# Kernel optimization log

Measured on AMD Instinct MI355X. Metric: run time of the kernel, lower is better.

Reference implementation:

```python
import jax, jax.numpy as jnp
import numpy as np

B, N, K = 4, 65536, 16
D_IN, D_OUT = 8, 16
DH = D_OUT // 2
GROUPS = 4  # GroupNorm: 4 groups since all channel counts here are < 64
NEG = 0.2   # LeakyReLU negative slope
EPS = 1e-5  # GroupNorm eps (torch default)


def _gather(feat, idx):
    # feat [B,C,N], idx [B,N,K] -> [B,C,N,K]  (gather_neighbour_V2)
    return jax.vmap(lambda f, i: f[:, i])(feat, idx)


def _gn(x, gamma, beta):
    b, c, n, k = x.shape
    xg = x.reshape(b, GROUPS, c // GROUPS, n, k)
    mu = xg.mean(axis=(2, 3, 4), keepdims=True)
    var = xg.var(axis=(2, 3, 4), keepdims=True)
    xg = (xg - mu) * jax.lax.rsqrt(var + EPS)
    return xg.reshape(b, c, n, k) * gamma[None, :, None, None] + beta[None, :, None, None]


def _mlp2d(x, W, bb, g, be, act=True):
    # Conv2d 1x1 (+bias) + GroupNorm + optional LeakyReLU(0.2)
    y = jnp.einsum('oc,bcnk->bonk', W, x) + bb[None, :, None, None]
    y = _gn(y, g, be)
    return jax.nn.leaky_relu(y, NEG) if act else y


def _att_pool(x, Wa, Wm, bm, gm, bem):
    # Att_pooling: 1x1 fc (no bias) -> softmax over nsample -> weighted sum -> MLP2D
    scores = jax.nn.softmax(jnp.einsum('oc,bcnk->bonk', Wa, x), axis=3)
    agg = jnp.sum(x * scores, axis=3, keepdims=True)  # [B,C,N,1]
    return _mlp2d(agg, Wm, bm, gm, bem)


def setup_inputs():
    key = jax.random.key(0)
    ks = list(jax.random.split(key, 16))
    def w(k, o, c):
        return jax.random.normal(k, (o, c), jnp.float32) * (2.0 / c) ** 0.5  # kaiming-ish
    inp = {
        'feature': jax.random.normal(ks[0], (B, D_IN, N, 1), jnp.float32),
        'xyz': jax.random.normal(ks[1], (B, 3, N), jnp.float32),
        'neigh_idx': jax.random.randint(ks[2], (B, N, K), 0, N),
        'W_mlp1': w(ks[3], DH, D_IN), 'b_mlp1': jnp.zeros(DH), 'g_mlp1': jnp.ones(DH), 'be_mlp1': jnp.zeros(DH),
        'W_lfa1': w(ks[4], DH, 10), 'b_lfa1': jnp.zeros(DH), 'g_lfa1': jnp.ones(DH), 'be_lfa1': jnp.zeros(DH),
        'Wa1': w(ks[5], D_OUT, D_OUT),
        'Wm1': w(ks[6], DH, D_OUT), 'bm1': jnp.zeros(DH), 'gm1': jnp.ones(DH), 'bem1': jnp.zeros(DH),
        'W_lfa2': w(ks[7], DH, DH), 'b_lfa2': jnp.zeros(DH), 'g_lfa2': jnp.ones(DH), 'be_lfa2': jnp.zeros(DH),
        'Wa2': w(ks[8], D_OUT, D_OUT),
        'Wm2': w(ks[9], D_OUT, D_OUT), 'bm2': jnp.zeros(D_OUT), 'gm2': jnp.ones(D_OUT), 'bem2': jnp.zeros(D_OUT),
        'W_mlp2': w(ks[10], 2 * D_OUT, D_OUT), 'b_mlp2': jnp.zeros(2 * D_OUT), 'g_mlp2': jnp.ones(2 * D_OUT), 'be_mlp2': jnp.zeros(2 * D_OUT),
        'W_skip': w(ks[11], 2 * D_OUT, D_IN), 'b_skip': jnp.zeros(2 * D_OUT), 'g_skip': jnp.ones(2 * D_OUT), 'be_skip': jnp.zeros(2 * D_OUT),
    }
    return inp


def reference(feature, xyz, neigh_idx,
              W_mlp1, b_mlp1, g_mlp1, be_mlp1,
              W_lfa1, b_lfa1, g_lfa1, be_lfa1,
              Wa1, Wm1, bm1, gm1, bem1,
              W_lfa2, b_lfa2, g_lfa2, be_lfa2,
              Wa2, Wm2, bm2, gm2, bem2,
              W_mlp2, b_mlp2, g_mlp2, be_mlp2,
              W_skip, b_skip, g_skip, be_skip):
    # Dilated_res_block.forward
    f_pc = _mlp2d(feature, W_mlp1, b_mlp1, g_mlp1, be_mlp1)          # [B,DH,N,1]
    # Building_block.relative_pos_encoding
    neigh_xyz = _gather(xyz, neigh_idx)                               # [B,3,N,K]
    xyz_tile = xyz[:, :, :, None]
    rel = neigh_xyz - xyz_tile
    dist = jnp.sqrt(jnp.sum(rel * rel, axis=1, keepdims=True))        # [B,1,N,K]
    f_rel = jnp.concatenate(
        [dist, rel, jnp.broadcast_to(xyz_tile, neigh_xyz.shape), neigh_xyz], axis=1)  # [B,10,N,K]
    f_xyz = _mlp2d(f_rel, W_lfa1, b_lfa1, g_lfa1, be_lfa1)            # [B,DH,N,K]
    f_neigh = _gather(f_pc[..., 0], neigh_idx)                        # [B,DH,N,K]
    f_concat = jnp.concatenate([f_neigh, f_xyz], axis=1)              # [B,D_OUT,N,K]
    f_agg = _att_pool(f_concat, Wa1, Wm1, bm1, gm1, bem1)             # [B,DH,N,1]
    f_xyz2 = _mlp2d(f_xyz, W_lfa2, b_lfa2, g_lfa2, be_lfa2)           # [B,DH,N,K]
    f_neigh2 = _gather(f_agg[..., 0], neigh_idx)                      # [B,DH,N,K]
    f_concat2 = jnp.concatenate([f_neigh2, f_xyz2], axis=1)           # [B,D_OUT,N,K]
    f_agg2 = _att_pool(f_concat2, Wa2, Wm2, bm2, gm2, bem2)           # [B,D_OUT,N,1]
    f_out = _mlp2d(f_agg2, W_mlp2, b_mlp2, g_mlp2, be_mlp2, act=False)    # [B,2*D_OUT,N,1]
    shortcut = _mlp2d(feature, W_skip, b_skip, g_skip, be_skip, act=False)
    return jax.nn.leaky_relu(f_out + shortcut, NEG)
```

## Files before the change

### kernel.cpp

```cpp
#include <hip/hip_runtime.h>
#include <hip/hip_bf16.h>

#define NPTS 65536
#define LOGN 16
#define KNB 16
#define NEGS 0.2f
#define EPSV 1e-5f

#define ST_MLP1 0
#define ST_SKIP 1
#define ST_L1   2
#define ST_M1   3
#define ST_L2   4
#define ST_M2   5
#define ST_OUT  6

#define STAT_F   14336
#define FIN_OFF  14336
#define RECA_OFF 16384
#define RECB_OFF  (RECA_OFF + 4*NPTS*8)
#define PREM2_OFF (RECB_OFF + 4*NPTS*8)
#define L2P_OFF   (PREM2_OFF + 4*NPTS*16)
#define L2P_FLOATS ((size_t)4*NPTS*KNB*4)
#define NEED_BYTES (((size_t)L2P_OFF + L2P_FLOATS)*4)

typedef __attribute__((ext_vector_type(8))) short short8;
typedef __attribute__((ext_vector_type(4))) float f32x4;
typedef __attribute__((ext_vector_type(4))) unsigned u32x4;

union U16 { uint4 u; short8 s; };

__device__ __forceinline__ float lrelu(float v){ return fmaxf(v, v*NEGS); }

__device__ __forceinline__ float s16(float v){ return v + __shfl_xor(v,16); }
__device__ __forceinline__ float s32(float v){ return v + __shfl_xor(v,32); }
__device__ __forceinline__ float x16max(float v){ return fmaxf(v, __shfl_xor(v,16)); }
__device__ __forceinline__ float x32max(float v){ return fmaxf(v, __shfl_xor(v,32)); }

__device__ __forceinline__ float wred(float v){
  #pragma unroll
  for(int off=32; off>0; off>>=1) v += __shfl_xor(v, off, 64);
  return v;
}

__device__ __forceinline__ void wave_fence(){
  __builtin_amdgcn_sched_barrier(0);
  asm volatile("s_waitcnt lgkmcnt(0)" ::: "memory");
  __builtin_amdgcn_sched_barrier(0);
}

__device__ __forceinline__ void load_fin(const float* fin, int stage, int b, int c,
                                         float& sc, float& sh){
  const float* fp = fin + ((stage*4+b)*32 + c)*2;
  sc = fp[0]; sh = fp[1];
}

__device__ __forceinline__ unsigned pkbf(float a, float b){
  __hip_bfloat162 h = __float22bfloat162_rn(make_float2(a,b));
  union{ __hip_bfloat162 h2; unsigned u; } cv; cv.h2 = h; return cv.u;
}
__device__ __forceinline__ float blo(unsigned d){ return __builtin_bit_cast(float, d<<16); }
__device__ __forceinline__ float bhi(unsigned d){ return __builtin_bit_cast(float, d & 0xffff0000u); }
__device__ __forceinline__ float bfu(unsigned short h){ return __builtin_bit_cast(float, ((unsigned)h)<<16); }

__device__ __forceinline__ int rowadr(int row){ return (row*16) ^ ((row&8)<<2); }

#define XB_OFF 0
#define AG_OFF 2048
#define WV_BYTES 2304

__device__ __forceinline__ void xcd_map(int bid, int& b, int& nblk){
  int xcd = bid & 7;
  b = xcd >> 1;
  nblk = ((bid >> 3) << 1) | (xcd & 1);
}

__global__ __launch_bounds__(256) void k_pack(const float* __restrict__ xyz,
                                              float* __restrict__ ws){
  int p = blockIdx.x*256 + threadIdx.x;
  int b = p >> LOGN, n = p & (NPTS-1);
  const float* xb = xyz + b*3*NPTS + n;
  float4 v = make_float4(xb[0], xb[NPTS], xb[2*NPTS], 0.f);
  *(float4*)((char*)(ws + RECA_OFF) + (size_t)p*32 + 16) = v;
  *(float4*)((char*)(ws + RECB_OFF) + (size_t)p*32 + 16) = v;
}

__device__ void fin_stage(const float* __restrict__ ws, float* __restrict__ fin,
                          int stage, int nch, float cnt,
                          const float* __restrict__ gamma, const float* __restrict__ beta){
  int t = threadIdx.x;
  if(t >= 4*nch) return;
  int b = t / nch, c = t - b*nch;
  int g = c / (nch/4);
  const float* sl = ws + ((stage*4+b)*4+g)*128;
  float s=0.f, q=0.f;
  #pragma unroll 8
  for(int i=0;i<64;i++){ s += sl[i]; q += sl[64+i]; }
  float mean = s/cnt;
  float var  = q/cnt - mean*mean;
  float inv  = rsqrtf(var + EPSV);
  float sc = inv*gamma[c];
  float sh = beta[c] - mean*sc;
  float* fp = fin + ((stage*4+b)*32 + c)*2;
  fp[0]=sc; fp[1]=sh;
}

__global__ __launch_bounds__(128) void kfA(float* __restrict__ ws,
    const float* g1, const float* be1, const float* gL1, const float* beL1,
    const float* gsk, const float* besk){
  if(blockIdx.x==0)      fin_stage(ws, ws+FIN_OFF, ST_MLP1, 8,  2.0f*NPTS,      g1, be1);
  else if(blockIdx.x==1) fin_stage(ws, ws+FIN_OFF, ST_L1,   8,  2.0f*NPTS*KNB,  gL1, beL1);
  else                   fin_stage(ws, ws+FIN_OFF, ST_SKIP, 32, 8.0f*NPTS,      gsk, besk);
}
__global__ __launch_bounds__(128) void kfB(float* __restrict__ ws,
    const float* gm1, const float* bem1, const float* gL2, const float* beL2){
  if(blockIdx.x==0) fin_stage(ws, ws+FIN_OFF, ST_M1, 8, 2.0f*NPTS,     gm1, bem1);
  else              fin_stage(ws, ws+FIN_OFF, ST_L2, 8, 2.0f*NPTS*KNB, gL2, beL2);
}
__global__ __launch_bounds__(128) void kfC(float* __restrict__ ws,
    const float* gm2, const float* bem2){
  fin_stage(ws, ws+FIN_OFF, ST_M2, 16, 4.0f*NPTS, gm2, bem2);
}
__global__ __launch_bounds__(128) void kfD(float* __restrict__ ws,
    const float* go, const float* beo){
  fin_stage(ws, ws+FIN_OFF, ST_OUT, 32, 8.0f*NPTS, go, beo);
}

__global__ __launch_bounds__(256) void k1(
    const float* __restrict__ feat, const int* __restrict__ nidx,
    const float* __restrict__ W1,  const float* __restrict__ b1,
    const float* __restrict__ Ws,  const float* __restrict__ bs,
    const float* __restrict__ WL1, const float* __restrict__ bl1,
    float* __restrict__ ws){
  int b, nblk; xcd_map(blockIdx.x, b, nblk);
  int n = nblk*256 + threadIdx.x;
  int p = (b<<LOGN) | n;
  char* recA = (char*)(ws + RECA_OFF);
  float f[8];
  #pragma unroll
  for(int c=0;c<8;c++) f[c] = __builtin_nontemporal_load(feat + (b*8+c)*NPTS + n);

  float s1s[4]={0,0,0,0}, s1q[4]={0,0,0,0};
  float pv[8];
  #pragma unroll
  for(int c=0;c<8;c++){
    float v = b1[c];
    #pragma unroll
    for(int j=0;j<8;j++) v += W1[c*8+j]*f[j];
    pv[c]=v;
    s1s[c>>1]+=v; s1q[c>>1]+=v*v;
  }
  uint4 pk = make_uint4(pkbf(pv[0],pv[1]), pkbf(pv[2],pv[3]),
                        pkbf(pv[4],pv[5]), pkbf(pv[6],pv[7]));
  *(uint4*)(recA + (size_t)p*32) = pk;

  float sss[4]={0,0,0,0}, ssq[4]={0,0,0,0};
  #pragma unroll
  for(int o=0;o<32;o++){
    float v = bs[o];
    #pragma unroll
    for(int j=0;j<8;j++) v += Ws[o*8+j]*f[j];
    sss[o>>3]+=v; ssq[o>>3]+=v*v;
  }
  float4 ct = *(const float4*)(recA + (size_t)p*32 + 16);
  float l1s[4]={0,0,0,0}, l1q[4]={0,0,0,0};
  const int* nr = nidx + p*KNB;
  #pragma unroll
  for(int k=0;k<KNB;k++){
    int idx = __builtin_nontemporal_load(nr + k);
    float4 nb = *(const float4*)(recA + ((size_t)((b<<LOGN)|idx))*32 + 16);
    float rx=nb.x-ct.x, ry=nb.y-ct.y, rz=nb.z-ct.z;
    float dd = __builtin_amdgcn_sqrtf(rx*rx+ry*ry+rz*rz);
    float fr[10] = {dd,rx,ry,rz,ct.x,ct.y,ct.z,nb.x,nb.y,nb.z};
    #pragma unroll
    for(int c=0;c<8;c++){
      float v = bl1[c];
      #pragma unroll
      for(int j=0;j<10;j++) v += WL1[c*10+j]*fr[j];
      l1s[c>>1]+=v; l1q[c>>1]+=v*v;
    }
  }
  __shared__ float lst[24];
  if(threadIdx.x < 24) lst[threadIdx.x] = 0.f;
  __syncthreads();
  int lane = threadIdx.x & 63;
  #pragma unroll
  for(int g=0; g<4; g++){
    float a1v = wred(s1s[g]), a2v = wred(s1q[g]);
    float d1v = wred(sss[g]), d2v = wred(ssq[g]);
    float e1v = wred(l1s[g]), e2v = wred(l1q[g]);
    if(lane==0){
      atomicAdd(&lst[ 0+g*2], a1v); atomicAdd(&lst[ 1+g*2], a2v);
      atomicAdd(&lst[ 8+g*2], d1v); atomicAdd(&lst[ 9+g*2], d2v);
      atomicAdd(&lst[16+g*2], e1v); atomicAdd(&lst[17+g*2], e2v);
    }
  }
  __syncthreads();
  if(threadIdx.x < 24){
    int stage = threadIdx.x >> 3;
    int g = (threadIdx.x >> 1) & 3;
    int w = threadIdx.x & 1;
    atomicAdd(ws + ((stage*4+b)*4+g)*128 + w*64 + (blockIdx.x&63), lst[threadIdx.x]);
  }
}

template<bool L2P>
__global__ __launch_bounds__(256,8) void k2(
    const int* __restrict__ nidx,
    const float* __restrict__ WL1, const float* __restrict__ bl1,
    const float* __restrict__ Wa1,
    const float* __restrict__ Wm1, const float* __restrict__ bm1,
    const float* __restrict__ W2,  const float* __restrict__ b2,
    float* __restrict__ ws){
  const float* fin = ws + FIN_OFF;
  int b, nblk; xcd_map(blockIdx.x, b, nblk);
  int tid = threadIdx.x;
  int w = tid>>6, lane = tid&63, q = lane>>4, l15 = lane&15;
  int nbase = nblk*16 + w*4;
  int pA = (b<<LOGN) | (nbase + q);

  float scP[8], shP[8], scL[8], shL[8];
  #pragma unroll
  for(int c=0;c<8;c++){
    load_fin(fin, ST_MLP1,b,c, scP[c],shP[c]);
    load_fin(fin, ST_L1,  b,c, scL[c],shL[c]);
  }
  U16 bu; bu.u = make_uint4(0,0,0,0);
  if(q < 2){
    const float* wr = Wa1 + l15*16 + q*8;
    float4 w0 = *(const float4*)(wr);
    float4 w1 = *(const float4*)(wr+4);
    bu.u = make_uint4(pkbf(w0.x,w0.y), pkbf(w0.z,w0.w), pkbf(w1.x,w1.y), pkbf(w1.z,w1.w));
  }

  __shared__ unsigned char SB[4][WV_BYTES];
  __shared__ float lst[16];
  if(tid<16) lst[tid]=0.f;
  char* wb = (char*)SB[w];

  char* recA = (char*)(ws + RECA_OFF);
  char* recB = (char*)(ws + RECB_OFF);

  int idx = __builtin_nontemporal_load(nidx + (size_t)pA*KNB + l15);
  const char* rp = recA + ((size_t)((b<<LOGN)|idx))*32;
  uint4 pk1  = *(const uint4*)(rp);
  float4 nb  = *(const float4*)(rp + 16);
  float4 ct  = *(const float4*)(recA + (size_t)pA*32 + 16);
  float rx=nb.x-ct.x, ry=nb.y-ct.y, rz=nb.z-ct.z;
  float dd = __builtin_amdgcn_sqrtf(rx*rx+ry*ry+rz*rz);
  float fr[10] = {dd,rx,ry,rz,ct.x,ct.y,ct.z,nb.x,nb.y,nb.z};
  float fx[8];
  #pragma unroll
  for(int c=0;c<8;c++){
    float v = bl1[c];
    #pragma unroll
    for(int j=0;j<10;j++) v += WL1[c*10+j]*fr[j];
    fx[c] = lrelu(v*scL[c]+shL[c]);
  }
  float xn[8];
  xn[0]=lrelu(blo(pk1.x)*scP[0]+shP[0]); xn[1]=lrelu(bhi(pk1.x)*scP[1]+shP[1]);
  xn[2]=lrelu(blo(pk1.y)*scP[2]+shP[2]); xn[3]=lrelu(bhi(pk1.y)*scP[3]+shP[3]);
  xn[4]=lrelu(blo(pk1.z)*scP[4]+shP[4]); xn[5]=lrelu(bhi(pk1.z)*scP[5]+shP[5]);
  xn[6]=lrelu(blo(pk1.w)*scP[6]+shP[6]); xn[7]=lrelu(bhi(pk1.w)*scP[7]+shP[7]);

  {
    uint4 d0 = make_uint4(pkbf(xn[0],xn[1]), pkbf(xn[2],xn[3]), pkbf(xn[4],xn[5]), pkbf(xn[6],xn[7]));
    uint4 d1 = make_uint4(pkbf(fx[0],fx[1]), pkbf(fx[2],fx[3]), pkbf(fx[4],fx[5]), pkbf(fx[6],fx[7]));
    char* base = wb + XB_OFF + q*256 + rowadr(l15);
    *(uint4*)(base)        = d0;
    *(uint4*)(base + 1024) = d1;
  }

  float l2v[8];
  #pragma unroll
  for(int c=0;c<8;c++){
    float v = b2[c];
    #pragma unroll
    for(int j=0;j<8;j++) v += W2[c*8+j]*fx[j];
    l2v[c]=v;
  }
  if constexpr (L2P){
    u32x4 lp = { pkbf(l2v[0],l2v[1]), pkbf(l2v[2],l2v[3]),
                 pkbf(l2v[4],l2v[5]), pkbf(l2v[6],l2v[7]) };
    __builtin_nontemporal_store(lp, (u32x4*)((char*)(ws + L2P_OFF) + ((size_t)pA*KNB + l15)*16));
  }

  wave_fence();

  f32x4 cz = {0.f,0.f,0.f,0.f};
  int rxf = q & 2;
  const char* xc = wb + XB_OFF + (l15>>3)*1024 + (l15&7)*2;
  #pragma unroll
  for(int pt=0; pt<4; pt++){
    U16 afr; afr.u = make_uint4(0,0,0,0);
    if(q < 2) afr.u = *(const uint4*)(wb + XB_OFF + q*1024 + pt*256 + rowadr(l15));
    f32x4 cf = __builtin_amdgcn_mfma_f32_16x16x32_bf16(afr.s, bu.s, cz, 0,0,0);
    float mx = fmaxf(fmaxf(cf[0],cf[1]), fmaxf(cf[2],cf[3]));
    mx = x16max(mx); mx = x32max(mx);
    float pe0=__expf(cf[0]-mx), pe1=__expf(cf[1]-mx), pe2=__expf(cf[2]-mx), pe3=__expf(cf[3]-mx);
    float ps = pe0+pe1+pe2+pe3;
    ps = s16(ps); ps = s32(ps);
    const char* xe = xc + pt*256 + 64*q;
    float acc = pe0*bfu(*(const unsigned short*)(xe + 16*(0^rxf)))
              + pe1*bfu(*(const unsigned short*)(xe + 16*(1^rxf)))
              + pe2*bfu(*(const unsigned short*)(xe + 16*(2^rxf)))
              + pe3*bfu(*(const unsigned short*)(xe + 16*(3^rxf)));
    acc = s16(acc); acc = s32(acc);
    float agg = acc*__builtin_amdgcn_rcpf(ps);
    if(q==0) *(float*)(wb + AG_OFF + (pt*16+l15)*4) = agg;
  }

  float l2s[4]={0,0,0,0}, l2q[4]={0,0,0,0};
  #pragma unroll
  for(int c=0;c<8;c++){ l2s[c>>1]+=l2v[c]; l2q[c>>1]+=l2v[c]*l2v[c]; }

  wave_fence();

  float m1v = 0.f;
  if(l15 < 8){
    const float4* agp = (const float4*)(wb + AG_OFF + q*64);
    float4 A0=agp[0], A1=agp[1], A2=agp[2], A3=agp[3];
    const float4* wp = (const float4*)(Wm1 + l15*16);
    float4 W0=wp[0], W1_=wp[1], W2_=wp[2], W3=wp[3];
    float v = bm1[l15];
    v += W0.x*A0.x + W0.y*A0.y + W0.z*A0.z + W0.w*A0.w;
    v += W1_.x*A1.x + W1_.y*A1.y + W1_.z*A1.z + W1_.w*A1.w;
    v += W2_.x*A2.x + W2_.y*A2.y + W2_.z*A2.z + W2_.w*A2.w;
    v += W3.x*A3.x + W3.y*A3.y + W3.z*A3.z + W3.w*A3.w;
    m1v = v;
  }
  float vpart = __shfl_xor(m1v, 1);
  if(l15 < 8 && (l15&1)==0){
    unsigned u = pkbf(m1v, vpart);
    int pD = (b<<LOGN) | (nbase + q);
    *(unsigned*)(recB + (size_t)pD*32 + (l15>>1)*4) = u;
  }
  float m1s = s16(m1v); m1s = s32(m1s); m1s += __shfl_xor(m1s,1);
  float m1qv = m1v*m1v;
  float m1q = s16(m1qv); m1q = s32(m1q); m1q += __shfl_xor(m1q,1);

  __syncthreads();
  #pragma unroll
  for(int g=0;g<4;g++){
    float a=wred(l2s[g]), qq=wred(l2q[g]);
    if(lane==0){ atomicAdd(&lst[g*2],a); atomicAdd(&lst[g*2+1],qq); }
  }
  if(lane < 8 && (lane&1)==0){
    atomicAdd(&lst[8+(lane>>1)*2],   m1s);
    atomicAdd(&lst[8+(lane>>1)*2+1], m1q);
  }
  __syncthreads();
  if(tid<16){
    int half=tid>>3, g=(tid>>1)&3, wsel=tid&1;
    int stage = half? ST_M1 : ST_L2;
    atomicAdd(ws + ((stage*4+b)*4+g)*128 + wsel*64 + (blockIdx.x&63), lst[tid]);
  }
}

template<bool L2P>
__global__ __launch_bounds__(256,8) void k3(
    const int* __restrict__ nidx,
    const float* __restrict__ WL1, const float* __restrict__ bl1,
    const float* __restrict__ W2,  const float* __restrict__ b2,
    const float* __restrict__ Wa2,
    const float* __restrict__ Wm2, const float* __restrict__ bm2,
    float* __restrict__ ws){
  const float* fin = ws + FIN_OFF;
  int b, nblk; xcd_map(blockIdx.x, b, nblk);
  int tid = threadIdx.x;
  int w = tid>>6, lane = tid&63, q = lane>>4, l15 = lane&15;
  int nbase = nblk*16 + w*4;
  int pA = (b<<LOGN) | (nbase + q);

  float scL[8], shL[8], scL2[8], shL2[8], scM[8], shM[8];
  #pragma unroll
  for(int c=0;c<8;c++){
    load_fin(fin, ST_L1, b,c, scL[c], shL[c]);
    load_fin(fin, ST_L2, b,c, scL2[c],shL2[c]);
    load_fin(fin, ST_M1, b,c, scM[c], shM[c]);
  }
  U16 bu; bu.u = make_uint4(0,0,0,0);
  if(q < 2){
    const float* wr = Wa2 + l15*16 + q*8;
    float4 w0 = *(const float4*)(wr);
    float4 w1 = *(const float4*)(wr+4);
    bu.u = make_uint4(pkbf(w0.x,w0.y), pkbf(w0.z,w0.w), pkbf(w1.x,w1.y), pkbf(w1.z,w1.w));
  }
  float wmr[16];
  {
    const float4* wp = (const float4*)(Wm2 + l15*16);
    float4 m0=wp[0], m1=wp[1], m2=wp[2], m3=wp[3];
    wmr[0]=m0.x; wmr[1]=m0.y; wmr[2]=m0.z; wmr[3]=m0.w;
    wmr[4]=m1.x; wmr[5]=m1.y; wmr[6]=m1.z; wmr[7]=m1.w;
    wmr[8]=m2.x; wmr[9]=m2.y; wmr[10]=m2.z; wmr[11]=m2.w;
    wmr[12]=m3.x; wmr[13]=m3.y; wmr[14]=m3.z; wmr[15]=m3.w;
  }

  __shared__ unsigned char SB[4][WV_BYTES];
  __shared__ float lst[8];
  if(tid<8) lst[tid]=0.f;
  char* wb = (char*)SB[w];

  char* recB = (char*)(ws + RECB_OFF);
  float* prem2 = ws + PREM2_OFF;

  int idx = __builtin_nontemporal_load(nidx + (size_t)pA*KNB + l15);
  const char* rp = recB + ((size_t)((b<<LOGN)|idx))*32;
  uint4 pm1 = *(const uint4*)(rp);
  float fx2[8];
  if constexpr (L2P){
    u32x4 lp = __builtin_nontemporal_load(
        (const u32x4*)((const char*)(ws + L2P_OFF) + ((size_t)pA*KNB + l15)*16));
    fx2[0]=lrelu(blo(lp.x)*scL2[0]+shL2[0]); fx2[1]=lrelu(bhi(lp.x)*scL2[1]+shL2[1]);
    fx2[2]=lrelu(blo(lp.y)*scL2[2]+shL2[2]); fx2[3]=lrelu(bhi(lp.y)*scL2[3]+shL2[3]);
    fx2[4]=lrelu(blo(lp.z)*scL2[4]+shL2[4]); fx2[5]=lrelu(bhi(lp.z)*scL2[5]+shL2[5]);
    fx2[6]=lrelu(blo(lp.w)*scL2[6]+shL2[6]); fx2[7]=lrelu(bhi(lp.w)*scL2[7]+shL2[7]);
  } else {
    float4 nb = *(const float4*)(rp + 16);
    float4 ct = *(const float4*)(recB + (size_t)pA*32 + 16);
    float rx=nb.x-ct.x, ry=nb.y-ct.y, rz=nb.z-ct.z;
    float dd = __builtin_amdgcn_sqrtf(rx*rx+ry*ry+rz*rz);
    float fr[10] = {dd,rx,ry,rz,ct.x,ct.y,ct.z,nb.x,nb.y,nb.z};
    float fx[8];
    #pragma unroll
    for(int c=0;c<8;c++){
      float v = bl1[c];
      #pragma unroll
      for(int j=0;j<10;j++) v += WL1[c*10+j]*fr[j];
      fx[c] = lrelu(v*scL[c]+shL[c]);
    }
    #pragma unroll
    for(int c=0;c<8;c++){
      float v = b2[c];
      #pragma unroll
      for(int j=0;j<8;j++) v += W2[c*8+j]*fx[j];
      fx2[c] = lrelu(v*scL2[c]+shL2[c]);
    }
  }
  float xn[8];
  xn[0]=lrelu(blo(pm1.x)*scM[0]+shM[0]); xn[1]=lrelu(bhi(pm1.x)*scM[1]+shM[1]);
  xn[2]=lrelu(blo(pm1.y)*scM[2]+shM[2]); xn[3]=lrelu(bhi(pm1.y)*scM[3]+shM[3]);
  xn[4]=lrelu(blo(pm1.z)*scM[4]+shM[4]); xn[5]=lrelu(bhi(pm1.z)*scM[5]+shM[5]);
  xn[6]=lrelu(blo(pm1.w)*scM[6]+shM[6]); xn[7]=lrelu(bhi(pm1.w)*scM[7]+shM[7]);

  {
    uint4 d0 = make_uint4(pkbf(xn[0],xn[1]), pkbf(xn[2],xn[3]), pkbf(xn[4],xn[5]), pkbf(xn[6],xn[7]));
    uint4 d1 = make_uint4(pkbf(fx2[0],fx2[1]), pkbf(fx2[2],fx2[3]), pkbf(fx2[4],fx2[5]), pkbf(fx2[6],fx2[7]));
    char* base = wb + XB_OFF + q*256 + rowadr(l15);
    *(uint4*)(base)        = d0;
    *(uint4*)(base + 1024) = d1;
  }

  wave_fence();

  f32x4 cz = {0.f,0.f,0.f,0.f};
  int rxf = q & 2;
  const char* xc = wb + XB_OFF + (l15>>3)*1024 + (l15&7)*2;
  #pragma unroll
  for(int pt=0; pt<4; pt++){
    U16 afr; afr.u = make_uint4(0,0,0,0);
    if(q < 2) afr.u = *(const uint4*)(wb + XB_OFF + q*1024 + pt*256 + rowadr(l15));
    f32x4 cf = __builtin_amdgcn_mfma_f32_16x16x32_bf16(afr.s, bu.s, cz, 0,0,0);
    float mx = fmaxf(fmaxf(cf[0],cf[1]), fmaxf(cf[2],cf[3]));
    mx = x16max(mx); mx = x32max(mx);
    float pe0=__expf(cf[0]-mx), pe1=__expf(cf[1]-mx), pe2=__expf(cf[2]-mx), pe3=__expf(cf[3]-mx);
    float ps = pe0+pe1+pe2+pe3;
    ps = s16(ps); ps = s32(ps);
    const char* xe = xc + pt*256 + 64*q;
    float acc = pe0*bfu(*(const unsigned short*)(xe + 16*(0^rxf)))
              + pe1*bfu(*(const unsigned short*)(xe + 16*(1^rxf)))
              + pe2*bfu(*(const unsigned short*)(xe + 16*(2^rxf)))
              + pe3*bfu(*(const unsigned short*)(xe + 16*(3^rxf)));
    acc = s16(acc); acc = s32(acc);
    float agg = acc*__builtin_amdgcn_rcpf(ps);
    if(q==0) *(float*)(wb + AG_OFF + (pt*16+l15)*4) = agg;
  }

  wave_fence();

  float v;
  {
    const float4* agp = (const float4*)(wb + AG_OFF + q*64);
    float4 A0=agp[0], A1=agp[1], A2=agp[2], A3=agp[3];
    v = bm2[l15];
    v += wmr[0]*A0.x + wmr[1]*A0.y + wmr[2]*A0.z + wmr[3]*A0.w;
    v += wmr[4]*A1.x + wmr[5]*A1.y + wmr[6]*A1.z + wmr[7]*A1.w;
    v += wmr[8]*A2.x + wmr[9]*A2.y + wmr[10]*A2.z + wmr[11]*A2.w;
    v += wmr[12]*A3.x + wmr[13]*A3.y + wmr[14]*A3.z + wmr[15]*A3.w;
  }
  int pD = (b<<LOGN) | (nbase + q);
  __builtin_nontemporal_store(v, prem2 + (size_t)pD*16 + l15);

  float s = s16(v);  s = s32(s);  s += __shfl_xor(s,1);  s += __shfl_xor(s,2);
  float qv = v*v;
  float qq = s16(qv); qq = s32(qq); qq += __shfl_xor(qq,1); qq += __shfl_xor(qq,2);

  __syncthreads();
  if(lane < 16 && (lane&3)==0){
    atomicAdd(&lst[(lane>>2)*2],   s);
    atomicAdd(&lst[(lane>>2)*2+1], qq);
  }
  __syncthreads();
  if(tid<8){
    int g=(tid>>1)&3, wsel=tid&1;
    atomicAdd(ws + ((ST_M2*4+b)*4+g)*128 + wsel*64 + (blockIdx.x&63), lst[tid]);
  }
}

__global__ __launch_bounds__(256) void k4(
    const float* __restrict__ Wo,  const float* __restrict__ bo,
    float* __restrict__ ws){
  const float* fin = ws + FIN_OFF;
  int b=blockIdx.y; int n=blockIdx.x*256+threadIdx.x; int p=(b<<LOGN)|n;
  float scM[16], shM[16];
  #pragma unroll
  for(int c=0;c<16;c++) load_fin(fin, ST_M2, b, c, scM[c], shM[c]);
  const f32x4* pm = (const f32x4*)(ws + PREM2_OFF) + (size_t)p*4;
  float fa[16];
  #pragma unroll
  for(int i=0;i<4;i++){
    f32x4 v4 = __builtin_nontemporal_load(pm + i);
    fa[i*4+0]=lrelu(v4.x*scM[i*4+0]+shM[i*4+0]);
    fa[i*4+1]=lrelu(v4.y*scM[i*4+1]+shM[i*4+1]);
    fa[i*4+2]=lrelu(v4.z*scM[i*4+2]+shM[i*4+2]);
    fa[i*4+3]=lrelu(v4.w*scM[i*4+3]+shM[i*4+3]);
  }
  float sos[4]={0,0,0,0}, soq[4]={0,0,0,0};
  #pragma unroll
  for(int o=0;o<32;o++){
    float v=bo[o];
    #pragma unroll
    for(int c=0;c<16;c++) v += Wo[o*16+c]*fa[c];
    sos[o>>3]+=v; soq[o>>3]+=v*v;
  }
  __shared__ float lst[8];
  if(threadIdx.x<8) lst[threadIdx.x]=0.f;
  __syncthreads();
  int lane = threadIdx.x & 63;
  #pragma unroll
  for(int g=0;g<4;g++){
    float a=wred(sos[g]), q=wred(soq[g]);
    if(lane==0){ atomicAdd(&lst[g*2],a); atomicAdd(&lst[g*2+1],q); }
  }
  __syncthreads();
  if(threadIdx.x<8){
    int g=(threadIdx.x>>1)&3, w=threadIdx.x&1;
    atomicAdd(ws + ((ST_OUT*4+b)*4+g)*128 + w*64 + (blockIdx.x&63), lst[threadIdx.x]);
  }
}

__global__ __launch_bounds__(256) void k5(
    const float* __restrict__ feat,
    const float* __restrict__ Wo,  const float* __restrict__ bo,
    const float* __restrict__ Wsk, const float* __restrict__ bsk,
    const float* __restrict__ ws, float* __restrict__ out){
  const float* fin = ws + FIN_OFF;
  int b=blockIdx.y; int n=blockIdx.x*256+threadIdx.x; int p=(b<<LOGN)|n;
  float scM[16], shM[16];
  #pragma unroll
  for(int c=0;c<16;c++) load_fin(fin, ST_M2, b, c, scM[c], shM[c]);
  const f32x4* pm = (const f32x4*)(ws + PREM2_OFF) + (size_t)p*4;
  float fa[16];
  #pragma unroll
  for(int i=0;i<4;i++){
    f32x4 v4 = __builtin_nontemporal_load(pm + i);
    fa[i*4+0]=lrelu(v4.x*scM[i*4+0]+shM[i*4+0]);
    fa[i*4+1]=lrelu(v4.y*scM[i*4+1]+shM[i*4+1]);
    fa[i*4+2]=lrelu(v4.z*scM[i*4+2]+shM[i*4+2]);
    fa[i*4+3]=lrelu(v4.w*scM[i*4+3]+shM[i*4+3]);
  }
  float f[8];
  #pragma unroll
  for(int c=0;c<8;c++) f[c]=__builtin_nontemporal_load(feat + (b*8+c)*NPTS + n);
  #pragma unroll
  for(int o=0;o<32;o++){
    float to = bo[o];
    #pragma unroll
    for(int c=0;c<16;c++) to += Wo[o*16+c]*fa[c];
    float ts = bsk[o];
    #pragma unroll
    for(int j=0;j<8;j++) ts += Wsk[o*8+j]*f[j];
    float scO, shO, scS, shS;
    load_fin(fin, ST_OUT,  b, o, scO, shO);
    load_fin(fin, ST_SKIP, b, o, scS, shS);
    float v = to*scO+shO + ts*scS+shS;
    __builtin_nontemporal_store(lrelu(v), out + (size_t)(b*32+o)*NPTS + n);
  }
}

extern "C" void kernel_launch(void* const* d_in, const int* in_sizes, int n_in,
                              void* d_out, int out_size, void* d_ws, size_t ws_size,
                              hipStream_t stream){
  (void)in_sizes; (void)n_in; (void)out_size;
  const float* feat=(const float*)d_in[0];
  const float* xyz =(const float*)d_in[1];
  const int*   nidx=(const int*)d_in[2];
  const float* W1  =(const float*)d_in[3];
  const float* b1  =(const float*)d_in[4];
  const float* g1  =(const float*)d_in[5];
  const float* be1 =(const float*)d_in[6];
  const float* WL1 =(const float*)d_in[7];
  const float* bl1 =(const float*)d_in[8];
  const float* gL1 =(const float*)d_in[9];
  const float* beL1=(const float*)d_in[10];
  const float* Wa1 =(const float*)d_in[11];
  const float* Wm1 =(const float*)d_in[12];
  const float* bm1 =(const float*)d_in[13];
  const float* gm1 =(const float*)d_in[14];
  const float* bem1=(const float*)d_in[15];
  const float* W2  =(const float*)d_in[16];
  const float* b2  =(const float*)d_in[17];
  const float* gL2 =(const float*)d_in[18];
  const float* beL2=(const float*)d_in[19];
  const float* Wa2 =(const float*)d_in[20];
  const float* Wm2 =(const float*)d_in[21];
  const float* bm2 =(const float*)d_in[22];
  const float* gm2 =(const float*)d_in[23];
  const float* bem2=(const float*)d_in[24];
  const float* Wo  =(const float*)d_in[25];
  const float* bo  =(const float*)d_in[26];
  const float* go  =(const float*)d_in[27];
  const float* beo =(const float*)d_in[28];
  const float* Wsk =(const float*)d_in[29];
  const float* bsk =(const float*)d_in[30];
  const float* gsk =(const float*)d_in[31];
  const float* besk=(const float*)d_in[32];
  float* ws=(float*)d_ws;
  float* out=(float*)d_out;

  bool useL2P = (ws_size >= NEED_BYTES);

  hipMemsetAsync(d_ws, 0, STAT_F*sizeof(float), stream);
  k_pack<<<dim3(1024),dim3(256),0,stream>>>(xyz, ws);
  k1<<<dim3(1024),dim3(256),0,stream>>>(feat, nidx, W1,b1, Wsk,bsk, WL1,bl1, ws);
  kfA<<<dim3(3),dim3(128),0,stream>>>(ws, g1,be1, gL1,beL1, gsk,besk);
  if(useL2P)
    k2<true><<<dim3(16384),dim3(256),0,stream>>>(nidx, WL1,bl1, Wa1, Wm1,bm1, W2,b2, ws);
  else
    k2<false><<<dim3(16384),dim3(256),0,stream>>>(nidx, WL1,bl1, Wa1, Wm1,bm1, W2,b2, ws);
  kfB<<<dim3(2),dim3(128),0,stream>>>(ws, gm1,bem1, gL2,beL2);
  if(useL2P)
    k3<true><<<dim3(16384),dim3(256),0,stream>>>(nidx, WL1,bl1, W2,b2, Wa2, Wm2,bm2, ws);
  else
    k3<false><<<dim3(16384),dim3(256),0,stream>>>(nidx, WL1,bl1, W2,b2, Wa2, Wm2,bm2, ws);
  kfC<<<dim3(1),dim3(128),0,stream>>>(ws, gm2,bem2);
  k4<<<dim3(256,4),dim3(256),0,stream>>>(Wo,bo, ws);
  kfD<<<dim3(1),dim3(128),0,stream>>>(ws, go,beo);
  k5<<<dim3(256,4),dim3(256),0,stream>>>(feat, Wo,bo, Wsk,bsk, ws, out);
}
```

Before: 261.9 us.

## Materialize lfa1 pre-activations in new pass and use permlane swaps for reductions

Splits k1 into a per-point kernel (mlp1 and skip stats) and a new per-pair kernel k1b that computes the lfa1 conv once, stores it as bf16 in a pair buffer and accumulates its GroupNorm stats. k2 then reads the stored values instead of re-gathering neighbour xyz and recomputing the 10->8 conv, and overwrites the same buffer with lfa2 pre-activations. Separately, cross-row shuffles in reductions use permlane16/32 swap builtins when available. The aim is to cut the recomputation and the scattered neighbour-xyz gathers. In exchange it adds a full pair-sized write and read pass (about 64 MB each way) plus an extra launch.

```diff
diff --git a/kernel.cpp b/kernel.cpp
--- a/kernel.cpp
+++ b/kernel.cpp
@@ -20,9 +20,9 @@
 #define RECA_OFF 16384
 #define RECB_OFF  (RECA_OFF + 4*NPTS*8)
 #define PREM2_OFF (RECB_OFF + 4*NPTS*8)
-#define L2P_OFF   (PREM2_OFF + 4*NPTS*16)
-#define L2P_FLOATS ((size_t)4*NPTS*KNB*4)
-#define NEED_BYTES (((size_t)L2P_OFF + L2P_FLOATS)*4)
+#define PAIR_OFF  (PREM2_OFF + 4*NPTS*16)
+#define PAIR_FLOATS ((size_t)4*NPTS*KNB*4)
+#define NEED_BYTES (((size_t)PAIR_OFF + PAIR_FLOATS)*4)
 
 typedef __attribute__((ext_vector_type(8))) short short8;
 typedef __attribute__((ext_vector_type(4))) float f32x4;
@@ -32,15 +32,55 @@
 
 __device__ __forceinline__ float lrelu(float v){ return fmaxf(v, v*NEGS); }
 
-__device__ __forceinline__ float s16(float v){ return v + __shfl_xor(v,16); }
-__device__ __forceinline__ float s32(float v){ return v + __shfl_xor(v,32); }
-__device__ __forceinline__ float x16max(float v){ return fmaxf(v, __shfl_xor(v,16)); }
-__device__ __forceinline__ float x32max(float v){ return fmaxf(v, __shfl_xor(v,32)); }
+#if defined(__has_builtin)
+#  if __has_builtin(__builtin_amdgcn_permlane32_swap)
+#    define HAVE_PL32 1
+#  endif
+#  if __has_builtin(__builtin_amdgcn_permlane16_swap)
+#    define HAVE_PL16 1
+#  endif
+#endif
+
+__device__ __forceinline__ float s16(float v){
+#ifdef HAVE_PL16
+  unsigned u = __builtin_bit_cast(unsigned, v);
+  auto r = __builtin_amdgcn_permlane16_swap(u, u, false, false);
+  return __builtin_bit_cast(float,(unsigned)r[0]) + __builtin_bit_cast(float,(unsigned)r[1]);
+#else
+  return v + __shfl_xor(v,16);
+#endif
+}
+__device__ __forceinline__ float s32(float v){
+#ifdef HAVE_PL32
+  unsigned u = __builtin_bit_cast(unsigned, v);
+  auto r = __builtin_amdgcn_permlane32_swap(u, u, false, false);
+  return __builtin_bit_cast(float,(unsigned)r[0]) + __builtin_bit_cast(float,(unsigned)r[1]);
+#else
+  return v + __shfl_xor(v,32);
+#endif
+}
+__device__ __forceinline__ float x16max(float v){
+#ifdef HAVE_PL16
+  unsigned u = __builtin_bit_cast(unsigned, v);
+  auto r = __builtin_amdgcn_permlane16_swap(u, u, false, false);
+  return fmaxf(__builtin_bit_cast(float,(unsigned)r[0]), __builtin_bit_cast(float,(unsigned)r[1]));
+#else
+  return fmaxf(v, __shfl_xor(v,16));
+#endif
+}
+__device__ __forceinline__ float x32max(float v){
+#ifdef HAVE_PL32
+  unsigned u = __builtin_bit_cast(unsigned, v);
+  auto r = __builtin_amdgcn_permlane32_swap(u, u, false, false);
+  return fmaxf(__builtin_bit_cast(float,(unsigned)r[0]), __builtin_bit_cast(float,(unsigned)r[1]));
+#else
+  return fmaxf(v, __shfl_xor(v,32));
+#endif
+}
 
 __device__ __forceinline__ float wred(float v){
-  #pragma unroll
-  for(int off=32; off>0; off>>=1) v += __shfl_xor(v, off, 64);
-  return v;
+  v += __shfl_xor(v,1); v += __shfl_xor(v,2); v += __shfl_xor(v,4); v += __shfl_xor(v,8);
+  v = s16(v); return s32(v);
 }
 
 __device__ __forceinline__ void wave_fence(){
@@ -126,7 +166,110 @@
   fin_stage(ws, ws+FIN_OFF, ST_OUT, 32, 8.0f*NPTS, go, beo);
 }
 
-__global__ __launch_bounds__(256) void k1(
+__global__ __launch_bounds__(256) void k1slim(
+    const float* __restrict__ feat,
+    const float* __restrict__ W1,  const float* __restrict__ b1,
+    const float* __restrict__ Ws,  const float* __restrict__ bs,
+    float* __restrict__ ws){
+  int b, nblk; xcd_map(blockIdx.x, b, nblk);
+  int n = nblk*256 + threadIdx.x;
+  int p = (b<<LOGN) | n;
+  char* recA = (char*)(ws + RECA_OFF);
+  float f[8];
+  #pragma unroll
+  for(int c=0;c<8;c++) f[c] = __builtin_nontemporal_load(feat + (b*8+c)*NPTS + n);
+
+  float s1s[4]={0,0,0,0}, s1q[4]={0,0,0,0};
+  float pv[8];
+  #pragma unroll
+  for(int c=0;c<8;c++){
+    float v = b1[c];
+    #pragma unroll
+    for(int j=0;j<8;j++) v += W1[c*8+j]*f[j];
+    pv[c]=v;
+    s1s[c>>1]+=v; s1q[c>>1]+=v*v;
+  }
+  uint4 pk = make_uint4(pkbf(pv[0],pv[1]), pkbf(pv[2],pv[3]),
+                        pkbf(pv[4],pv[5]), pkbf(pv[6],pv[7]));
+  *(uint4*)(recA + (size_t)p*32) = pk;
+
+  float sss[4]={0,0,0,0}, ssq[4]={0,0,0,0};
+  #pragma unroll
+  for(int o=0;o<32;o++){
+    float v = bs[o];
+    #pragma unroll
+    for(int j=0;j<8;j++) v += Ws[o*8+j]*f[j];
+    sss[o>>3]+=v; ssq[o>>3]+=v*v;
+  }
+  __shared__ float lst[16];
+  if(threadIdx.x < 16) lst[threadIdx.x] = 0.f;
+  __syncthreads();
+  int lane = threadIdx.x & 63;
+  #pragma unroll
+  for(int g=0; g<4; g++){
+    float a1v = wred(s1s[g]), a2v = wred(s1q[g]);
+    float d1v = wred(sss[g]), d2v = wred(ssq[g]);
+    if(lane==0){
+      atomicAdd(&lst[0+g*2], a1v); atomicAdd(&lst[1+g*2], a2v);
+      atomicAdd(&lst[8+g*2], d1v); atomicAdd(&lst[9+g*2], d2v);
+    }
+  }
+  __syncthreads();
+  if(threadIdx.x < 16){
+    int stage = (threadIdx.x < 8) ? ST_MLP1 : ST_SKIP;
+    int g = (threadIdx.x >> 1) & 3;
+    int w = threadIdx.x & 1;
+    atomicAdd(ws + ((stage*4+b)*4+g)*128 + w*64 + (blockIdx.x&63), lst[threadIdx.x]);
+  }
+}
+
+__global__ __launch_bounds__(256,8) void k1b(
+    const int* __restrict__ nidx,
+    const float* __restrict__ WL1, const float* __restrict__ bl1,
+    float* __restrict__ ws){
+  int b, nblk; xcd_map(blockIdx.x, b, nblk);
+  int tid = threadIdx.x;
+  int lane = tid&63, q = (lane>>4), l15 = lane&15;
+  int nbase = nblk*16 + (tid>>6)*4;
+  int pA = (b<<LOGN) | (nbase + q);
+  char* recA = (char*)(ws + RECA_OFF);
+  char* pairb = (char*)(ws + PAIR_OFF);
+
+  int idx = __builtin_nontemporal_load(nidx + (size_t)pA*KNB + l15);
+  float4 nb = *(const float4*)(recA + ((size_t)((b<<LOGN)|idx))*32 + 16);
+  float4 ct = *(const float4*)(recA + (size_t)pA*32 + 16);
+  float rx=nb.x-ct.x, ry=nb.y-ct.y, rz=nb.z-ct.z;
+  float dd = __builtin_amdgcn_sqrtf(rx*rx+ry*ry+rz*rz);
+  float fr[10] = {dd,rx,ry,rz,ct.x,ct.y,ct.z,nb.x,nb.y,nb.z};
+  float lv[8];
+  float l1s[4]={0,0,0,0}, l1q[4]={0,0,0,0};
+  #pragma unroll
+  for(int c=0;c<8;c++){
+    float v = bl1[c];
+    #pragma unroll
+    for(int j=0;j<10;j++) v += WL1[c*10+j]*fr[j];
+    lv[c]=v;
+    l1s[c>>1]+=v; l1q[c>>1]+=v*v;
+  }
+  u32x4 lp = { pkbf(lv[0],lv[1]), pkbf(lv[2],lv[3]), pkbf(lv[4],lv[5]), pkbf(lv[6],lv[7]) };
+  __builtin_nontemporal_store(lp, (u32x4*)(pairb + ((size_t)pA*KNB + l15)*16));
+
+  __shared__ float lst[8];
+  if(tid<8) lst[tid]=0.f;
+  __syncthreads();
+  #pragma unroll
+  for(int g=0;g<4;g++){
+    float a=wred(l1s[g]), qq=wred(l1q[g]);
+    if(lane==0){ atomicAdd(&lst[g*2],a); atomicAdd(&lst[g*2+1],qq); }
+  }
+  __syncthreads();
+  if(tid<8){
+    int g=(tid>>1)&3, w=tid&1;
+    atomicAdd(ws + ((ST_L1*4+b)*4+g)*128 + w*64 + (blockIdx.x&63), lst[tid]);
+  }
+}
+
+__global__ __launch_bounds__(256) void k1full(
     const float* __restrict__ feat, const int* __restrict__ nidx,
     const float* __restrict__ W1,  const float* __restrict__ b1,
     const float* __restrict__ Ws,  const float* __restrict__ bs,
@@ -204,7 +347,7 @@
   }
 }
 
-template<bool L2P>
+template<bool PAIR>
 __global__ __launch_bounds__(256,8) void k2(
     const int* __restrict__ nidx,
     const float* __restrict__ WL1, const float* __restrict__ bl1,
@@ -240,22 +383,32 @@
 
   char* recA = (char*)(ws + RECA_OFF);
   char* recB = (char*)(ws + RECB_OFF);
+  char* pairb = (char*)(ws + PAIR_OFF);
 
   int idx = __builtin_nontemporal_load(nidx + (size_t)pA*KNB + l15);
   const char* rp = recA + ((size_t)((b<<LOGN)|idx))*32;
   uint4 pk1  = *(const uint4*)(rp);
-  float4 nb  = *(const float4*)(rp + 16);
-  float4 ct  = *(const float4*)(recA + (size_t)pA*32 + 16);
-  float rx=nb.x-ct.x, ry=nb.y-ct.y, rz=nb.z-ct.z;
-  float dd = __builtin_amdgcn_sqrtf(rx*rx+ry*ry+rz*rz);
-  float fr[10] = {dd,rx,ry,rz,ct.x,ct.y,ct.z,nb.x,nb.y,nb.z};
   float fx[8];
-  #pragma unroll
-  for(int c=0;c<8;c++){
-    float v = bl1[c];
-    #pragma unroll
-    for(int j=0;j<10;j++) v += WL1[c*10+j]*fr[j];
-    fx[c] = lrelu(v*scL[c]+shL[c]);
+  if constexpr (PAIR){
+    u32x4 lp = __builtin_nontemporal_load(
+        (const u32x4*)(pairb + ((size_t)pA*KNB + l15)*16));
+    fx[0]=lrelu(blo(lp.x)*scL[0]+shL[0]); fx[1]=lrelu(bhi(lp.x)*scL[1]+shL[1]);
+    fx[2]=lrelu(blo(lp.y)*scL[2]+shL[2]); fx[3]=lrelu(bhi(lp.y)*scL[3]+shL[3]);
+    fx[4]=lrelu(blo(lp.z)*scL[4]+shL[4]); fx[5]=lrelu(bhi(lp.z)*scL[5]+shL[5]);
+    fx[6]=lrelu(blo(lp.w)*scL[6]+shL[6]); fx[7]=lrelu(bhi(lp.w)*scL[7]+shL[7]);
+  } else {
+    float4 nb  = *(const float4*)(rp + 16);
+    float4 ct  = *(const float4*)(recA + (size_t)pA*32 + 16);
+    float rx=nb.x-ct.x, ry=nb.y-ct.y, rz=nb.z-ct.z;
+    float dd = __builtin_amdgcn_sqrtf(rx*rx+ry*ry+rz*rz);
+    float fr[10] = {dd,rx,ry,rz,ct.x,ct.y,ct.z,nb.x,nb.y,nb.z};
+    #pragma unroll
+    for(int c=0;c<8;c++){
+      float v = bl1[c];
+      #pragma unroll
+      for(int j=0;j<10;j++) v += WL1[c*10+j]*fr[j];
+      fx[c] = lrelu(v*scL[c]+shL[c]);
+    }
   }
   float xn[8];
   xn[0]=lrelu(blo(pk1.x)*scP[0]+shP[0]); xn[1]=lrelu(bhi(pk1.x)*scP[1]+shP[1]);
@@ -279,10 +432,10 @@
     for(int j=0;j<8;j++) v += W2[c*8+j]*fx[j];
     l2v[c]=v;
   }
-  if constexpr (L2P){
-    u32x4 lp = { pkbf(l2v[0],l2v[1]), pkbf(l2v[2],l2v[3]),
-                 pkbf(l2v[4],l2v[5]), pkbf(l2v[6],l2v[7]) };
-    __builtin_nontemporal_store(lp, (u32x4*)((char*)(ws + L2P_OFF) + ((size_t)pA*KNB + l15)*16));
+  if constexpr (PAIR){
+    u32x4 lp2 = { pkbf(l2v[0],l2v[1]), pkbf(l2v[2],l2v[3]),
+                  pkbf(l2v[4],l2v[5]), pkbf(l2v[6],l2v[7]) };
+    __builtin_nontemporal_store(lp2, (u32x4*)(pairb + ((size_t)pA*KNB + l15)*16));
   }
 
   wave_fence();
@@ -357,7 +510,7 @@
   }
 }
 
-template<bool L2P>
+template<bool PAIR>
 __global__ __launch_bounds__(256,8) void k3(
     const int* __restrict__ nidx,
     const float* __restrict__ WL1, const float* __restrict__ bl1,
@@ -402,15 +555,16 @@
   char* wb = (char*)SB[w];
 
   char* recB = (char*)(ws + RECB_OFF);
+  char* pairb = (char*)(ws + PAIR_OFF);
   float* prem2 = ws + PREM2_OFF;
 
   int idx = __builtin_nontemporal_load(nidx + (size_t)pA*KNB + l15);
   const char* rp = recB + ((size_t)((b<<LOGN)|idx))*32;
   uint4 pm1 = *(const uint4*)(rp);
   float fx2[8];
-  if constexpr (L2P){
+  if constexpr (PAIR){
     u32x4 lp = __builtin_nontemporal_load(
-        (const u32x4*)((const char*)(ws + L2P_OFF) + ((size_t)pA*KNB + l15)*16));
+        (const u32x4*)(pairb + ((size_t)pA*KNB + l15)*16));
     fx2[0]=lrelu(blo(lp.x)*scL2[0]+shL2[0]); fx2[1]=lrelu(bhi(lp.x)*scL2[1]+shL2[1]);
     fx2[2]=lrelu(blo(lp.y)*scL2[2]+shL2[2]); fx2[3]=lrelu(bhi(lp.y)*scL2[3]+shL2[3]);
     fx2[4]=lrelu(blo(lp.z)*scL2[4]+shL2[4]); fx2[5]=lrelu(bhi(lp.z)*scL2[5]+shL2[5]);
@@ -628,18 +782,23 @@
   float* ws=(float*)d_ws;
   float* out=(float*)d_out;
 
-  bool useL2P = (ws_size >= NEED_BYTES);
+  bool usePair = (ws_size >= NEED_BYTES);
 
   hipMemsetAsync(d_ws, 0, STAT_F*sizeof(float), stream);
   k_pack<<<dim3(1024),dim3(256),0,stream>>>(xyz, ws);
-  k1<<<dim3(1024),dim3(256),0,stream>>>(feat, nidx, W1,b1, Wsk,bsk, WL1,bl1, ws);
+  if(usePair){
+    k1b<<<dim3(16384),dim3(256),0,stream>>>(nidx, WL1,bl1, ws);
+    k1slim<<<dim3(1024),dim3(256),0,stream>>>(feat, W1,b1, Wsk,bsk, ws);
+  } else {
+    k1full<<<dim3(1024),dim3(256),0,stream>>>(feat, nidx, W1,b1, Wsk,bsk, WL1,bl1, ws);
+  }
   kfA<<<dim3(3),dim3(128),0,stream>>>(ws, g1,be1, gL1,beL1, gsk,besk);
-  if(useL2P)
+  if(usePair)
     k2<true><<<dim3(16384),dim3(256),0,stream>>>(nidx, WL1,bl1, Wa1, Wm1,bm1, W2,b2, ws);
   else
     k2<false><<<dim3(16384),dim3(256),0,stream>>>(nidx, WL1,bl1, Wa1, Wm1,bm1, W2,b2, ws);
   kfB<<<dim3(2),dim3(128),0,stream>>>(ws, gm1,bem1, gL2,beL2);
-  if(useL2P)
+  if(usePair)
     k3<true><<<dim3(16384),dim3(256),0,stream>>>(nidx, WL1,bl1, W2,b2, Wa2, Wm2,bm2, ws);
   else
     k3<false><<<dim3(16384),dim3(256),0,stream>>>(nidx, WL1,bl1, W2,b2, Wa2, Wm2,bm2, ws);
```

After: 265.2 us. Within noise of the previous version (+1.3%).
